# Performance work log

Hardware: AMD Instinct MI355X
Metric: run time of the kernel (lower is better)

The kernel has to match this reference:

```python
import jax, jax.numpy as jnp
import numpy as np

L = 4            # l1 = l2 = lambd = 4
M = 2 * L + 1    # 9 m-channels
N = 4096         # environment pairs
D = 256          # feature channels
K = 100          # number of nonzero real-CG terms


def setup_inputs() -> dict:
    key = jax.random.key(0)
    k1, k2, k3, k4, k5, k6 = jax.random.split(key, 6)
    X1 = jax.random.normal(k1, (M, N, D), dtype=jnp.float32)
    X2 = jax.random.normal(k2, (M, N, D), dtype=jnp.float32)
    m1_aligned = jax.random.randint(k3, (K,), 0, M)
    m2_aligned = jax.random.randint(k4, (K,), 0, M)
    mu = jnp.sort(jax.random.randint(k5, (K,), 0, M))  # appended in mu order in the torch init
    multipliers = jax.random.normal(k6, (K,), dtype=jnp.float32)
    return {"X1": X1, "X2": X2, "m1_aligned": m1_aligned,
            "m2_aligned": m2_aligned, "mu": mu, "multipliers": multipliers}


def reference(X1, X2, m1_aligned, m2_aligned, mu, multipliers):
    # gather along m-dim, elementwise multiply by CG multipliers  -> [K, N, D]
    contributions = X1[m1_aligned] * X2[m2_aligned] * multipliers[:, None, None]
    # scatter-add into the 2*lambd+1 output channels (mu is sorted)
    result = jax.ops.segment_sum(contributions, mu, num_segments=M,
                                 indices_are_sorted=True)
    return result  # [2*lambd+1, N, D]
```

## Files before the change

### kernel.cpp

```cpp
#include <hip/hip_runtime.h>


#define M_CH 9
#define CSIZE 768

__global__ __launch_bounds__(64) void prep_kernel(
    const int* __restrict__ m1, const int* __restrict__ m2,
    const int* __restrict__ mu, const float* __restrict__ mult,
    int K, float* __restrict__ Cd) {
    if (threadIdx.x == 0) {
        for (int i = 0; i < CSIZE; ++i) Cd[i] = 0.f;
        for (int k = 0; k < K; ++k) {
            const int idx = (m1[k] * M_CH + m2[k]) * M_CH + mu[k];
            Cd[idx] += mult[k];
        }
    }
}

__global__ __launch_bounds__(64) void cleb_dense(
    const float* __restrict__ X1, const float* __restrict__ X2,
    const float* __restrict__ Cd, float* __restrict__ out, int P) {
    const int lane = threadIdx.x;
    const size_t base = (size_t)blockIdx.x * 256 + (size_t)lane * 4;

    float4 x1[M_CH], x2[M_CH];
    #pragma unroll
    for (int m = 0; m < M_CH; ++m) {
        x1[m] = *(const float4*)(X1 + (size_t)m * P + base);
        x2[m] = *(const float4*)(X2 + (size_t)m * P + base);
    }

    int tab[12];
    #pragma unroll
    for (int r = 0; r < 12; ++r)
        tab[r] = ((const int*)Cd)[r * 64 + lane];

    float4 acc[M_CH];
    #pragma unroll
    for (int m = 0; m < M_CH; ++m) acc[m] = make_float4(0.f, 0.f, 0.f, 0.f);

    #pragma unroll
    for (int p1 = 0; p1 < M_CH; ++p1) {
        #pragma unroll
        for (int p2 = 0; p2 < M_CH; ++p2) {
            float4 prod;
            prod.x = x1[p1].x * x2[p2].x;
            prod.y = x1[p1].y * x2[p2].y;
            prod.z = x1[p1].z * x2[p2].z;
            prod.w = x1[p1].w * x2[p2].w;
            #pragma unroll
            for (int m = 0; m < M_CH; ++m) {
                const int idx = (p1 * M_CH + p2) * M_CH + m;
                const float c = __int_as_float(
                    __builtin_amdgcn_readlane(tab[idx >> 6], idx & 63));
                acc[m].x = fmaf(c, prod.x, acc[m].x);
                acc[m].y = fmaf(c, prod.y, acc[m].y);
                acc[m].z = fmaf(c, prod.z, acc[m].z);
                acc[m].w = fmaf(c, prod.w, acc[m].w);
            }
        }
    }

    #pragma unroll
    for (int m = 0; m < M_CH; ++m)
        *(float4*)(out + (size_t)m * P + base) = acc[m];
}

extern "C" void kernel_launch(void* const* d_in, const int* in_sizes, int n_in,
                              void* d_out, int out_size, void* d_ws, size_t ws_size,
                              hipStream_t stream) {
    const float* X1   = (const float*)d_in[0];
    const float* X2   = (const float*)d_in[1];
    const int*   m1   = (const int*)d_in[2];
    const int*   m2   = (const int*)d_in[3];
    const int*   mu   = (const int*)d_in[4];
    const float* mult = (const float*)d_in[5];
    float* out = (float*)d_out;
    float* Cd  = (float*)d_ws;

    const int K = in_sizes[2];
    const int P = in_sizes[0] / M_CH;

    prep_kernel<<<1, 64, 0, stream>>>(m1, m2, mu, mult, K, Cd);
    cleb_dense<<<P / 256, 64, 0, stream>>>(X1, X2, Cd, out, P);
}
```

Measured before the change: 149.8 us.

## Parallelize CG table prep with atomics and pack FMAs into float2 vectors

The prep kernel now zeroes the dense CG table with 128 threads and accumulates the K terms with one atomicAdd per thread, instead of running both loops on a single thread. The main kernel reads coefficients directly from global memory (uniform scalar loads) rather than staging them in registers and using readlane. It also restructures the math into float2 vector FMAs so the compiler can emit packed FP32 instructions. Risks: the approach assumes K ≤ 128, and the scalar-load path may add latency compared with the readlane approach.

```diff
diff --git a/kernel.cpp b/kernel.cpp
--- a/kernel.cpp
+++ b/kernel.cpp
@@ -4,16 +4,18 @@
 #define M_CH 9
 #define CSIZE 768
 
-__global__ __launch_bounds__(64) void prep_kernel(
+typedef float v2f __attribute__((ext_vector_type(2)));
+
+__global__ __launch_bounds__(128) void prep_kernel(
     const int* __restrict__ m1, const int* __restrict__ m2,
     const int* __restrict__ mu, const float* __restrict__ mult,
     int K, float* __restrict__ Cd) {
-    if (threadIdx.x == 0) {
-        for (int i = 0; i < CSIZE; ++i) Cd[i] = 0.f;
-        for (int k = 0; k < K; ++k) {
-            const int idx = (m1[k] * M_CH + m2[k]) * M_CH + mu[k];
-            Cd[idx] += mult[k];
-        }
+    const int t = threadIdx.x;
+    for (int i = t; i < CSIZE; i += 128) Cd[i] = 0.f;
+    __syncthreads();
+    if (t < K) {
+        const int idx = (m1[t] * M_CH + m2[t]) * M_CH + mu[t];
+        atomicAdd(&Cd[idx], mult[t]);
     }
 }
 
@@ -23,47 +25,42 @@
     const int lane = threadIdx.x;
     const size_t base = (size_t)blockIdx.x * 256 + (size_t)lane * 4;
 
-    float4 x1[M_CH], x2[M_CH];
+    v2f x1[M_CH][2], x2[M_CH][2];
     #pragma unroll
     for (int m = 0; m < M_CH; ++m) {
-        x1[m] = *(const float4*)(X1 + (size_t)m * P + base);
-        x2[m] = *(const float4*)(X2 + (size_t)m * P + base);
+        const float4 a = *(const float4*)(X1 + (size_t)m * P + base);
+        const float4 b = *(const float4*)(X2 + (size_t)m * P + base);
+        x1[m][0] = (v2f){a.x, a.y}; x1[m][1] = (v2f){a.z, a.w};
+        x2[m][0] = (v2f){b.x, b.y}; x2[m][1] = (v2f){b.z, b.w};
     }
 
-    int tab[12];
+    v2f acc[M_CH][2];
     #pragma unroll
-    for (int r = 0; r < 12; ++r)
-        tab[r] = ((const int*)Cd)[r * 64 + lane];
-
-    float4 acc[M_CH];
-    #pragma unroll
-    for (int m = 0; m < M_CH; ++m) acc[m] = make_float4(0.f, 0.f, 0.f, 0.f);
+    for (int m = 0; m < M_CH; ++m) { acc[m][0] = (v2f)0.f; acc[m][1] = (v2f)0.f; }
 
     #pragma unroll
     for (int p1 = 0; p1 < M_CH; ++p1) {
         #pragma unroll
         for (int p2 = 0; p2 < M_CH; ++p2) {
-            float4 prod;
-            prod.x = x1[p1].x * x2[p2].x;
-            prod.y = x1[p1].y * x2[p2].y;
-            prod.z = x1[p1].z * x2[p2].z;
-            prod.w = x1[p1].w * x2[p2].w;
+            const v2f prod0 = x1[p1][0] * x2[p2][0];
+            const v2f prod1 = x1[p1][1] * x2[p2][1];
             #pragma unroll
             for (int m = 0; m < M_CH; ++m) {
-                const int idx = (p1 * M_CH + p2) * M_CH + m;
-                const float c = __int_as_float(
-                    __builtin_amdgcn_readlane(tab[idx >> 6], idx & 63));
-                acc[m].x = fmaf(c, prod.x, acc[m].x);
-                acc[m].y = fmaf(c, prod.y, acc[m].y);
-                acc[m].z = fmaf(c, prod.z, acc[m].z);
-                acc[m].w = fmaf(c, prod.w, acc[m].w);
+                const float c = Cd[(p1 * M_CH + p2) * M_CH + m];
+                const v2f cv = (v2f){c, c};
+                acc[m][0] = __builtin_elementwise_fma(cv, prod0, acc[m][0]);
+                acc[m][1] = __builtin_elementwise_fma(cv, prod1, acc[m][1]);
             }
         }
     }
 
     #pragma unroll
-    for (int m = 0; m < M_CH; ++m)
-        *(float4*)(out + (size_t)m * P + base) = acc[m];
+    for (int m = 0; m < M_CH; ++m) {
+        float4 r;
+        r.x = acc[m][0].x; r.y = acc[m][0].y;
+        r.z = acc[m][1].x; r.w = acc[m][1].y;
+        *(float4*)(out + (size_t)m * P + base) = r;
+    }
 }
 
 extern "C" void kernel_launch(void* const* d_in, const int* in_sizes, int n_in,
@@ -81,6 +78,6 @@
     const int K = in_sizes[2];
     const int P = in_sizes[0] / M_CH;
 
-    prep_kernel<<<1, 64, 0, stream>>>(m1, m2, mu, mult, K, Cd);
+    prep_kernel<<<1, 128, 0, stream>>>(m1, m2, mu, mult, K, Cd);
     cleb_dense<<<P / 256, 64, 0, stream>>>(X1, X2, Cd, out, P);
 }
```

New measurement: 127.2 us. -15.1%, faster.
